# Optimization experiments

Measured on AMD Instinct MI355X. Metric: run time of the kernel, lower is better.

Reference implementation:

```python
import jax, jax.numpy as jnp
import numpy as np

N, E, T = 20000, 320000, 64
INP, EMB, OUT = 128, 16, 3
HEADS, MSIZE, MDIM, KDIM, VDIM = 4, 1024, 128, 64, 64


def setup_inputs() -> dict:
    key = jax.random.key(0)
    ks = iter(jax.random.split(key, 64))

    def nrm(shape, s=0.05):
        return jax.random.normal(next(ks), shape, dtype=jnp.float32) * s

    return dict(
        x=jax.random.normal(next(ks), (N, INP), dtype=jnp.float32),
        edge_index=jax.random.randint(next(ks), (2, E), 0, N),
        index=5,
        inp_types=jax.random.randint(next(ks), (T,), 0, 4),
        log_return=jax.random.normal(next(ks), (T,), dtype=jnp.float32),
        # SAGEConv 1 (SoftmaxAggregation temp t1, lin_l/lin_r, bias=False)
        t1=jnp.ones((1, INP), jnp.float32),
        W1l=nrm((INP, 512)), W1r=nrm((INP, 512)),
        ln1g_w=jnp.ones((512,), jnp.float32), ln1g_b=jnp.zeros((512,), jnp.float32),
        # SAGEConv 2
        t2=jnp.ones((1, 512), jnp.float32),
        W2l=nrm((512, 256)), W2r=nrm((512, 256)),
        ln2g_w=jnp.ones((256,), jnp.float32), ln2g_b=jnp.zeros((256,), jnp.float32),
        # MemPooling(256,128,heads=4,num_clusters=1)
        mp_k=nrm((HEADS, 1, 256), 1.0),
        mp_conv=nrm((HEADS,), 0.5),            # Conv2d(heads,1,1,bias=False)
        mp_lin=nrm((256, 128)),                # Linear(in,out,bias=False)
        fxg_w=nrm((128, 256)), fxg_b=jnp.zeros((256,), jnp.float32),
        # PolicyNet head
        emb=nrm((4, EMB), 1.0),
        fk_w=nrm((256, KDIM)), fk_b=jnp.zeros((KDIM,), jnp.float32),
        fv_w=nrm((256, VDIM)), fv_b=jnp.zeros((VDIM,), jnp.float32),
        # MultiHeadMemory
        mem=nrm((HEADS, MSIZE, MDIM), 1.0),
        mfk_w=nrm((MDIM, KDIM)), mfk_b=jnp.zeros((KDIM,), jnp.float32),
        mfv_w=nrm((MDIM, VDIM)), mfv_b=jnp.zeros((VDIM,), jnp.float32),
        mfx_w=nrm((VDIM * HEADS, VDIM)), mfx_b=jnp.zeros((VDIM,), jnp.float32),
        f1_w=nrm((INP + EMB + 2 * VDIM + 1, 512)),
        n1_w=jnp.ones((512,), jnp.float32), n1_b=jnp.zeros((512,), jnp.float32),
        f2_w=nrm((512, 256)),
        n2_w=jnp.ones((256,), jnp.float32), n2_b=jnp.zeros((256,), jnp.float32),
        f3_w=nrm((256, OUT)), f3_b=jnp.zeros((OUT,), jnp.float32),
    )


def _forward(x, t1, W1l, W1r, ln1g_w, ln1g_b, t2, W2l, W2r, ln2g_w, ln2g_b,
             mp_k, mp_conv, mp_lin, fxg_w, fxg_b, emb, fk_w, fk_b, fv_w, fv_b,
             mem, mfk_w, mfk_b, mfv_w, mfv_b, mfx_w, mfx_b,
             f1_w, n1_w, n1_b, f2_w, n2_w, n2_b, f3_w, f3_b,
             log_return, edge_index, inp_types, index):
    n = x.shape[0]
    src, dst = edge_index[0], edge_index[1]

    def sage(h, t, Wl, Wr):
        hj = h[src]                                    # [E, C] gather
        gate = hj * t                                  # learned softmax temperature
        m = jax.ops.segment_max(gate, dst, num_segments=n)
        e = jnp.exp(gate - m[dst])                     # segment-stable softmax
        s = jax.ops.segment_sum(e, dst, num_segments=n)
        agg = jax.ops.segment_sum(hj * (e / s[dst]), dst, num_segments=n)
        return agg @ Wl + h @ Wr                       # SAGEConv, bias=False

    def graph_ln(h, w, b, eps=1e-5):                   # PyG LayerNorm, mode='graph'
        hc = h - jnp.mean(h)
        return hc / jnp.sqrt(jnp.mean(hc * hc) + eps) * w + b

    h = jax.nn.relu(graph_ln(sage(x, t1, W1l, W1r), ln1g_w, ln1g_b))
    h = jax.nn.relu(graph_ln(sage(h, t2, W2l, W2r), ln2g_w, ln2g_b))

    # MemPooling (single graph => B=1), tau=1: student-t kernel over sq. distances
    H, K, C = mp_k.shape
    kk = mp_k.reshape(H * K, C)
    d2 = jnp.maximum(jnp.sum(kk * kk, 1)[:, None] - 2.0 * (kk @ h.T)
                     + jnp.sum(h * h, 1)[None, :], 0.0)        # [H*K, N]
    dist = 1.0 / (1.0 + d2)
    dist = dist.reshape(H, K, n).transpose(0, 2, 1)[None]      # [1, H, N, K]
    S = dist / jnp.sum(dist, -1, keepdims=True)
    S = jax.nn.softmax(jnp.einsum('h,bhnk->bnk', mp_conv, S), axis=-1)  # [1, N, K]
    zp = jnp.einsum('bnk,nc->bkc', S, h)[:, 0, :]              # squeeze(1), K==1
    z = (zp @ mp_lin) @ fxg_w + fxg_b                          # [1, 256]

    q = jax.nn.softmax(z @ fk_w + fk_b, axis=-1)               # [1, key_dim]
    v = z @ fv_w + fv_b                                        # [1, val_dim]

    # MultiHeadMemory
    km = jax.nn.softmax(mem @ mfk_w + mfk_b, axis=-1)          # [H, M, key]
    vm = mem @ mfv_w + mfv_b                                   # [H, M, val]
    w = jax.nn.softmax(jnp.einsum('bk,hnk->bhn', q, km), axis=-1)
    mv = jnp.einsum('bhn,hnv->bhv', w, vm).reshape(q.shape[0], -1)
    m_out = mv @ mfx_w + mfx_b                                 # [1, val]

    zz = jnp.concatenate([v, m_out], axis=-1)                  # [1, 2*val]
    t_len = inp_types.shape[0]
    xi = jnp.broadcast_to(x[index][None, :], (t_len, x.shape[1]))
    zb = jnp.broadcast_to(zz, (t_len, zz.shape[1]))
    feat = jnp.concatenate([xi, emb[inp_types], log_return.reshape(-1, 1), zb], axis=-1)

    def ln(h2, w2, b2, eps=1e-5):                              # nn.LayerNorm (last dim)
        mu = jnp.mean(h2, -1, keepdims=True)
        hc = h2 - mu
        return hc / jnp.sqrt(jnp.mean(hc * hc, -1, keepdims=True) + eps) * w2 + b2

    h1 = jax.nn.relu(ln(feat @ f1_w, n1_w, n1_b))              # dropout = identity (eval)
    h2 = jax.nn.relu(ln(h1 @ f2_w, n2_w, n2_b))
    return jax.nn.softmax(h2 @ f3_w + f3_b, axis=-1)           # [T, out_dim]


def reference(x, edge_index, index, inp_types, log_return, t1, W1l, W1r, ln1g_w, ln1g_b,
              t2, W2l, W2r, ln2g_w, ln2g_b, mp_k, mp_conv, mp_lin, fxg_w, fxg_b, emb,
              fk_w, fk_b, fv_w, fv_b, mem, mfk_w, mfk_b, mfv_w, mfv_b, mfx_w, mfx_b,
              f1_w, n1_w, n1_b, f2_w, n2_w, n2_b, f3_w, f3_b):
    return _forward(x, t1, W1l, W1r, ln1g_w, ln1g_b, t2, W2l, W2r, ln2g_w, ln2g_b,
                    mp_k, mp_conv, mp_lin, fxg_w, fxg_b, emb, fk_w, fk_b, fv_w, fv_b,
                    mem, mfk_w, mfk_b, mfv_w, mfv_b, mfx_w, mfx_b,
                    f1_w, n1_w, n1_b, f2_w, n2_w, n2_b, f3_w, f3_b,
                    log_return, edge_index, inp_types, index)
```

## Files before the change

kernel.cpp:

```cpp
#include <hip/hip_runtime.h>

typedef __attribute__((ext_vector_type(8))) short bf16x8;
typedef __attribute__((ext_vector_type(8))) unsigned short ushort8_t;
typedef __attribute__((ext_vector_type(4))) float f32x4;

__device__ __forceinline__ unsigned short f2bf(float f) {
    unsigned int x = __float_as_uint(f);
    unsigned int r = x + 0x7fffu + ((x >> 16) & 1u);
    return (unsigned short)(r >> 16);
}
__device__ __forceinline__ float bf2f(unsigned short u) {
    return __uint_as_float(((unsigned int)u) << 16);
}
__device__ __forceinline__ float fexp2(float x) { return __builtin_amdgcn_exp2f(x); }

#define LOG2E 1.44269504089f

__global__ __launch_bounds__(256) void prep_kernel(
    const int* __restrict__ dst, int E, int* __restrict__ counts,
    const float* __restrict__ x, unsigned short* __restrict__ xb, size_t nx4,
    const float* __restrict__ W1l, const float* __restrict__ W1r, unsigned short* __restrict__ Bt1,
    const float* __restrict__ W2l, const float* __restrict__ W2r, unsigned short* __restrict__ Bt2) {
    int i = blockIdx.x * 256 + threadIdx.x;
    int total = gridDim.x * 256;
    if (i < E) atomicAdd(&counts[dst[i]], 1);
    for (size_t j = i; j < nx4; j += total) {
        float4 v = *(const float4*)(x + j * 4);
        ushort4 o;
        o.x = f2bf(v.x); o.y = f2bf(v.y); o.z = f2bf(v.z); o.w = f2bf(v.w);
        *(ushort4*)(xb + j * 4) = o;
    }
    if (i < 512 * 256) {
        int nn = i >> 8, k = i & 255;
        float v = (k < 128) ? W1l[(size_t)k * 512 + nn] : W1r[(size_t)(k - 128) * 512 + nn];
        Bt1[i] = f2bf(v);
    }
    if (i < 256 * 1024) {
        int nn = i >> 10, k = i & 1023;
        float v = (k < 512) ? W2l[(size_t)k * 256 + nn] : W2r[(size_t)(k - 512) * 256 + nn];
        Bt2[i] = f2bf(v);
    }
}

template <int CHUNK>
__global__ __launch_bounds__(1024) void scan_kernel(int* __restrict__ cnt,
                                                    int* __restrict__ off, int n) {
    __shared__ int s[1024];
    int tid = threadIdx.x;
    int base = tid * CHUNK;
    int loc[CHUNK];
    int sum = 0;
#pragma unroll
    for (int i = 0; i < CHUNK; ++i) {
        int idx = base + i;
        int v = 0;
        if (idx < n) { v = cnt[idx]; cnt[idx] = 0; }
        sum += v;
        loc[i] = sum;
    }
    s[tid] = sum;
    __syncthreads();
    for (int d = 1; d < 1024; d <<= 1) {
        int t = (tid >= d) ? s[tid - d] : 0;
        __syncthreads();
        s[tid] += t;
        __syncthreads();
    }
    int prev = (tid > 0) ? s[tid - 1] : 0;
    if (tid == 0) off[0] = 0;
#pragma unroll
    for (int i = 0; i < CHUNK; ++i) {
        int idx = base + i;
        if (idx < n) off[idx + 1] = prev + loc[i];
    }
}

__global__ void fill_kernel(const int* __restrict__ src, const int* __restrict__ dst, int E,
                            const int* __restrict__ off, int* __restrict__ cursor,
                            int* __restrict__ srcs) {
    int i = blockIdx.x * 256 + threadIdx.x;
    if (i < E) {
        int d = dst[i];
        int p = atomicAdd(&cursor[d], 1);
        srcs[off[d] + p] = src[i];
    }
}

__global__ __launch_bounds__(256) void agg512(const unsigned short* __restrict__ h,
                                              const float* __restrict__ t,
                                              const int* __restrict__ off,
                                              const int* __restrict__ srcs,
                                              unsigned short* __restrict__ agg, int n) {
    int wid = threadIdx.x >> 6, lane = threadIdx.x & 63;
    int node = blockIdx.x * 4 + wid;
    if (node >= n) return;
    int beg = off[node], end = off[node + 1];
    int col = lane * 8;
    float tc[8], sE[8], sW[8];
#pragma unroll
    for (int i = 0; i < 8; ++i) { tc[i] = t[col + i] * LOG2E; sE[i] = 0.f; sW[i] = 0.f; }
#define P8(u)                                       \
    _Pragma("unroll") for (int i = 0; i < 8; ++i) { \
        float v = bf2f(u[i]);                       \
        float wv = fexp2(v * tc[i]);                \
        sE[i] += wv; sW[i] += v * wv;               \
    }
    int e = beg;
    for (; e + 2 <= end; e += 2) {
        int s0 = srcs[e], s1 = srcs[e + 1];
        ushort8_t u0 = *(const ushort8_t*)(h + (size_t)s0 * 512 + col);
        ushort8_t u1 = *(const ushort8_t*)(h + (size_t)s1 * 512 + col);
        P8(u0) P8(u1)
    }
    if (e < end) {
        int s0 = srcs[e];
        ushort8_t u0 = *(const ushort8_t*)(h + (size_t)s0 * 512 + col);
        P8(u0)
    }
#undef P8
    ushort8_t o;
#pragma unroll
    for (int i = 0; i < 8; ++i) o[i] = f2bf((end > beg) ? (sW[i] / sE[i]) : 0.f);
    *(ushort8_t*)(agg + (size_t)node * 512 + col) = o;
}

__global__ __launch_bounds__(256) void agg128(const unsigned short* __restrict__ h,
                                              const float* __restrict__ t,
                                              const int* __restrict__ off,
                                              const int* __restrict__ srcs,
                                              unsigned short* __restrict__ agg, int n) {
    int wid = threadIdx.x >> 6, lane = threadIdx.x & 63;
    int node = blockIdx.x * 4 + wid;
    if (node >= n) return;
    int beg = off[node], end = off[node + 1];
    int col = lane * 2;
    float t0 = t[col] * LOG2E, t1 = t[col + 1] * LOG2E;
    float e0 = 0.f, e1 = 0.f, w0 = 0.f, w1 = 0.f;
#define P2(u)                                          \
    {                                                  \
        float a = bf2f(u.x), b = bf2f(u.y);            \
        float xa = fexp2(a * t0), xb = fexp2(b * t1);  \
        e0 += xa; e1 += xb; w0 += a * xa; w1 += b * xb; \
    }
    int e = beg;
    for (; e + 4 <= end; e += 4) {
        ushort2 u0 = *(const ushort2*)(h + (size_t)srcs[e] * 128 + col);
        ushort2 u1 = *(const ushort2*)(h + (size_t)srcs[e + 1] * 128 + col);
        ushort2 u2 = *(const ushort2*)(h + (size_t)srcs[e + 2] * 128 + col);
        ushort2 u3 = *(const ushort2*)(h + (size_t)srcs[e + 3] * 128 + col);
        P2(u0) P2(u1) P2(u2) P2(u3)
    }
    for (; e < end; ++e) {
        ushort2 u0 = *(const ushort2*)(h + (size_t)srcs[e] * 128 + col);
        P2(u0)
    }
#undef P2
    ushort2 o;
    o.x = f2bf((end > beg) ? (w0 / e0) : 0.f);
    o.y = f2bf((end > beg) ? (w1 / e1) : 0.f);
    *(ushort2*)(agg + (size_t)node * 128 + col) = o;
}

__global__ __launch_bounds__(256) void gemm_dual_mfma3(
    const unsigned short* __restrict__ A1, const unsigned short* __restrict__ A2,
    const unsigned short* __restrict__ Bt,
    unsigned short* __restrict__ Cb, double* __restrict__ part,
    int M, int N, int K1, int K2) {
    const int Kc = K1 + K2;
    __shared__ unsigned short As[64 * 40];
    __shared__ unsigned short Bs[256 * 40];
    __shared__ double rs[256], rs2[256];
    int tid = threadIdx.x;
    int lane = tid & 63, w = tid >> 6;
    int m0 = blockIdx.y * 64, n0 = blockIdx.x * 256;
    f32x4 acc[4][4] = {};
    int kg = lane >> 4, lr = lane & 15;

    for (int k0 = 0; k0 < Kc; k0 += 32) {
        const unsigned short* Asrc;
        int kk, Ksrc;
        if (k0 < K1) { Asrc = A1; kk = k0; Ksrc = K1; }
        else         { Asrc = A2; kk = k0 - K1; Ksrc = K2; }
        {
            int r = tid >> 2, ch = tid & 3;
            int gr = m0 + r;
            ushort8_t v = {0, 0, 0, 0, 0, 0, 0, 0};
            if (gr < M) v = *(const ushort8_t*)(Asrc + (size_t)gr * Ksrc + kk + ch * 8);
            *(ushort8_t*)&As[r * 40 + ch * 8] = v;
        }
#pragma unroll
        for (int it = 0; it < 4; ++it) {
            int idx = tid + it * 256;
            int r = idx >> 2, ch = idx & 3;
            const unsigned short* srcp = Bt + (size_t)(n0 + r) * Kc + k0 + ch * 8;
            *(ushort8_t*)&Bs[r * 40 + ch * 8] = *(const ushort8_t*)srcp;
        }
        __syncthreads();
        bf16x8 a[4], b[4];
#pragma unroll
        for (int i = 0; i < 4; ++i)
            a[i] = *(bf16x8*)&As[(i * 16 + lr) * 40 + kg * 8];
#pragma unroll
        for (int j = 0; j < 4; ++j)
            b[j] = *(bf16x8*)&Bs[(w * 64 + j * 16 + lr) * 40 + kg * 8];
#pragma unroll
        for (int i = 0; i < 4; ++i)
#pragma unroll
            for (int j = 0; j < 4; ++j)
                acc[i][j] = __builtin_amdgcn_mfma_f32_16x16x32_bf16(a[i], b[j], acc[i][j], 0, 0, 0);
        __syncthreads();
    }
    double s = 0, s2 = 0;
#pragma unroll
    for (int i = 0; i < 4; ++i) {
        int rbase = m0 + i * 16 + kg * 4;
#pragma unroll
        for (int j = 0; j < 4; ++j) {
            int col = n0 + w * 64 + j * 16 + lr;
#pragma unroll
            for (int reg = 0; reg < 4; ++reg) {
                int row = rbase + reg;
                if (row < M) {
                    float v = acc[i][j][reg];
                    Cb[(size_t)row * N + col] = f2bf(v);
                    s += v;
                    s2 += (double)v * v;
                }
            }
        }
    }
    rs[tid] = s;
    rs2[tid] = s2;
    __syncthreads();
    for (int d = 128; d; d >>= 1) {
        if (tid < d) { rs[tid] += rs[tid + d]; rs2[tid] += rs2[tid + d]; }
        __syncthreads();
    }
    if (tid == 0) {
        int bid = blockIdx.y * gridDim.x + blockIdx.x;
        part[bid * 2] = rs[0];
        part[bid * 2 + 1] = rs2[0];
    }
}

template <int C>
__global__ __launch_bounds__(256) void ln_relu_ip(unsigned short* __restrict__ z,
                                                  const float* __restrict__ w,
                                                  const float* __restrict__ b,
                                                  const double* __restrict__ part, int nb,
                                                  float invn, size_t n) {
    __shared__ float st[2];
    if (threadIdx.x < 64) {
        double s = 0, s2 = 0;
        for (int i = threadIdx.x; i < nb; i += 64) { s += part[2 * i]; s2 += part[2 * i + 1]; }
        for (int d = 32; d; d >>= 1) { s += __shfl_down(s, d); s2 += __shfl_down(s2, d); }
        if (threadIdx.x == 0) {
            float mu = (float)(s * invn);
            float var = (float)(s2 * invn) - mu * mu;
            st[0] = mu;
            st[1] = rsqrtf(var + 1e-5f);
        }
    }
    __syncthreads();
    float mu = st[0], inv = st[1];
    size_t stride = (size_t)gridDim.x * 256 * 4;
    for (size_t i = ((size_t)blockIdx.x * 256 + threadIdx.x) * 4; i < n; i += stride) {
        ushort4 v = *(const ushort4*)(z + i);
        int c = (int)(i & (C - 1));
        ushort4 o;
        o.x = f2bf(fmaxf((bf2f(v.x) - mu) * inv * w[c] + b[c], 0.f));
        o.y = f2bf(fmaxf((bf2f(v.y) - mu) * inv * w[c + 1] + b[c + 1], 0.f));
        o.z = f2bf(fmaxf((bf2f(v.z) - mu) * inv * w[c + 2] + b[c + 2], 0.f));
        o.w = f2bf(fmaxf((bf2f(v.w) - mu) * inv * w[c + 3] + b[c + 3], 0.f));
        *(ushort4*)(z + i) = o;
    }
}

__global__ __launch_bounds__(256) void ln_colsum(const unsigned short* __restrict__ z2,
                                                 const float* __restrict__ w,
                                                 const float* __restrict__ b,
                                                 const double* __restrict__ part, int nb,
                                                 float invn, int n,
                                                 float* __restrict__ cspartT) {
    __shared__ float red[8 * 256];
    __shared__ float st[2];
    int tid = threadIdx.x;
    if (tid < 64) {
        double s = 0, s2 = 0;
        for (int i = tid; i < nb; i += 64) { s += part[2 * i]; s2 += part[2 * i + 1]; }
        for (int d = 32; d; d >>= 1) { s += __shfl_down(s, d); s2 += __shfl_down(s2, d); }
        if (tid == 0) {
            float mu = (float)(s * invn);
            float var = (float)(s2 * invn) - mu * mu;
            st[0] = mu;
            st[1] = rsqrtf(var + 1e-5f);
        }
    }
    __syncthreads();
    float mu = st[0], inv = st[1];
    int cg = tid & 31;
    int rl = tid >> 5;
    int c8 = cg * 8;
    float lw[8], lb[8];
#pragma unroll
    for (int i = 0; i < 8; ++i) { lw[i] = w[c8 + i] * inv; lb[i] = b[c8 + i] - mu * inv * w[c8 + i]; }
    int rows_per = (n + gridDim.x - 1) / gridDim.x;
    int r0 = blockIdx.x * rows_per;
    int r1 = min(n, r0 + rows_per);
    float acc[8] = {};
    for (int r = r0 + rl; r < r1; r += 8) {
        ushort8_t u = *(const ushort8_t*)(z2 + (size_t)r * 256 + c8);
#pragma unroll
        for (int i = 0; i < 8; ++i) acc[i] += fmaxf(bf2f(u[i]) * lw[i] + lb[i], 0.f);
    }
#pragma unroll
    for (int i = 0; i < 8; ++i) red[rl * 256 + c8 + i] = acc[i];
    __syncthreads();
    float s = 0;
#pragma unroll
    for (int r = 0; r < 8; ++r) s += red[r * 256 + tid];
    cspartT[tid * 64 + blockIdx.x] = s;
}

__global__ __launch_bounds__(256) void zqv_kernel(const float* __restrict__ cspartT,
                                                  const float* __restrict__ mp_lin,
                                                  const float* __restrict__ fxg_w,
                                                  const float* __restrict__ fxg_b,
                                                  const float* __restrict__ fk_w,
                                                  const float* __restrict__ fk_b,
                                                  const float* __restrict__ fv_w,
                                                  const float* __restrict__ fv_b,
                                                  float* __restrict__ qv) {
    __shared__ float zp_s[256], u_s[128], z_s[256], ql_s[64];
    __shared__ float part_s[1024];
    int tid = threadIdx.x;
    {
        float s = 0;
        const float* p = cspartT + tid * 64;
#pragma unroll
        for (int i = 0; i < 16; ++i) {
            float4 v = *(const float4*)(p + i * 4);
            s += v.x + v.y + v.z + v.w;
        }
        zp_s[tid] = s;
    }
    __syncthreads();
    {
        int og = tid & 31, kc = tid >> 5;
        int j4 = og * 4;
        f32x4 a = {0.f, 0.f, 0.f, 0.f};
        for (int ci = 0; ci < 32; ++ci) {
            int c = kc * 32 + ci;
            float4 w = *(const float4*)(mp_lin + (size_t)c * 128 + j4);
            float zc = zp_s[c];
            a[0] += zc * w.x; a[1] += zc * w.y; a[2] += zc * w.z; a[3] += zc * w.w;
        }
#pragma unroll
        for (int i = 0; i < 4; ++i) part_s[kc * 128 + j4 + i] = a[i];
    }
    __syncthreads();
    if (tid < 128) {
        float s = 0;
#pragma unroll
        for (int kc = 0; kc < 8; ++kc) s += part_s[kc * 128 + tid];
        u_s[tid] = s;
    }
    __syncthreads();
    {
        int og = tid & 63, kc = tid >> 6;
        int j4 = og * 4;
        f32x4 a = {0.f, 0.f, 0.f, 0.f};
        for (int ci = 0; ci < 32; ++ci) {
            int c = kc * 32 + ci;
            float4 w = *(const float4*)(fxg_w + (size_t)c * 256 + j4);
            float uc = u_s[c];
            a[0] += uc * w.x; a[1] += uc * w.y; a[2] += uc * w.z; a[3] += uc * w.w;
        }
#pragma unroll
        for (int i = 0; i < 4; ++i) part_s[kc * 256 + j4 + i] = a[i];
    }
    __syncthreads();
    {
        float s = fxg_b[tid];
#pragma unroll
        for (int kc = 0; kc < 4; ++kc) s += part_s[kc * 256 + tid];
        z_s[tid] = s;
    }
    __syncthreads();
    {
        int og = tid & 15, kc = tid >> 4;
        int j4 = og * 4;
        f32x4 a = {0.f, 0.f, 0.f, 0.f};
        for (int ci = 0; ci < 16; ++ci) {
            int c = kc * 16 + ci;
            float4 w = *(const float4*)(fk_w + (size_t)c * 64 + j4);
            float zc = z_s[c];
            a[0] += zc * w.x; a[1] += zc * w.y; a[2] += zc * w.z; a[3] += zc * w.w;
        }
#pragma unroll
        for (int i = 0; i < 4; ++i) part_s[kc * 64 + j4 + i] = a[i];
    }
    __syncthreads();
    if (tid < 64) {
        float s = fk_b[tid];
#pragma unroll
        for (int kc = 0; kc < 16; ++kc) s += part_s[kc * 64 + tid];
        ql_s[tid] = s;
    }
    __syncthreads();
    {
        int og = tid & 15, kc = tid >> 4;
        int j4 = og * 4;
        f32x4 a = {0.f, 0.f, 0.f, 0.f};
        for (int ci = 0; ci < 16; ++ci) {
            int c = kc * 16 + ci;
            float4 w = *(const float4*)(fv_w + (size_t)c * 64 + j4);
            float zc = z_s[c];
            a[0] += zc * w.x; a[1] += zc * w.y; a[2] += zc * w.z; a[3] += zc * w.w;
        }
#pragma unroll
        for (int i = 0; i < 4; ++i) part_s[kc * 64 + j4 + i] = a[i];
    }
    __syncthreads();
    if (tid < 64) {
        float mx = ql_s[tid];
        for (int d = 32; d; d >>= 1) mx = fmaxf(mx, __shfl_xor(mx, d));
        float e = __expf(ql_s[tid] - mx);
        float s = e;
        for (int d = 32; d; d >>= 1) s += __shfl_xor(s, d);
        qv[tid] = e / s;
        float vv = fv_b[tid];
#pragma unroll
        for (int kc = 0; kc < 16; ++kc) vv += part_s[kc * 64 + tid];
        qv[64 + tid] = vv;
    }
}

__global__ __launch_bounds__(256) void mem_kv_logit(const float* __restrict__ mem,
                                                    const float* __restrict__ mfk_w,
                                                    const float* __restrict__ mfk_b,
                                                    const float* __restrict__ mfv_w,
                                                    const float* __restrict__ mfv_b,
                                                    const float* __restrict__ qv,
                                                    float* __restrict__ logits,
                                                    float* __restrict__ vm) {
    __shared__ float rows[4][128];
    __shared__ float qs[64];
    int tid = threadIdx.x;
    int r0 = blockIdx.x * 4;
    if (tid < 64) qs[tid] = qv[tid];
    for (int i = tid; i < 512; i += 256) rows[i >> 7][i & 127] = mem[(size_t)r0 * 128 + i];
    __syncthreads();
    int lr = tid >> 6;
    int lane = tid & 63;
    const float* row = rows[lr];
    float kl = mfk_b[lane], vl = mfv_b[lane];
#pragma unroll 8
    for (int c = 0; c < 128; ++c) {
        float rv = row[c];
        kl += rv * mfk_w[c * 64 + lane];
        vl += rv * mfv_w[c * 64 + lane];
    }
    float mx = kl;
    for (int d = 32; d; d >>= 1) mx = fmaxf(mx, __shfl_xor(mx, d));
    float e = __expf(kl - mx);
    float s = e;
    for (int d = 32; d; d >>= 1) s += __shfl_xor(s, d);
    float kval = e / s;
    float wl = kval * qs[lane];
    for (int d = 32; d; d >>= 1) wl += __shfl_xor(wl, d);
    size_t gr = (size_t)(r0 + lr);
    if (lane == 0) logits[gr] = wl;
    vm[gr * 64 + lane] = vl;
}

__global__ __launch_bounds__(256) void attend_part(const float* __restrict__ logits,
                                                   const float* __restrict__ vm,
                                                   float* __restrict__ part) {
    int b = blockIdx.x;
    int h = b >> 4;
    int s0 = (b & 15) * 64;
    int tid = threadIdx.x;
    __shared__ float els[64];
    __shared__ float pr[4][64];
    __shared__ float lmax_s, lsum_s;
    if (tid < 64) {
        float lg = logits[h * 1024 + s0 + tid];
        float m = lg;
        for (int d = 32; d; d >>= 1) m = fmaxf(m, __shfl_xor(m, d));
        float e = __expf(lg - m);
        els[tid] = e;
        float s = e;
        for (int d = 32; d; d >>= 1) s += __shfl_xor(s, d);
        if (tid == 0) { lmax_s = m; lsum_s = s; }
    }
    __syncthreads();
    int dd = tid & 63, g = tid >> 6;
    float acc = 0;
    for (int s = g; s < 64; s += 4)
        acc += els[s] * vm[((size_t)h * 1024 + s0 + s) * 64 + dd];
    pr[g][dd] = acc;
    __syncthreads();
    if (tid < 64) {
        float pv = pr[0][tid] + pr[1][tid] + pr[2][tid] + pr[3][tid];
        part[b * 66 + 2 + tid] = pv;
        if (tid == 0) { part[b * 66] = lmax_s; part[b * 66 + 1] = lsum_s; }
    }
}

__global__ __launch_bounds__(256) void attend_final(const float* __restrict__ part,
                                                    const float* __restrict__ mfx_w,
                                                    const float* __restrict__ mfx_b,
                                                    float* __restrict__ m_out) {
    __shared__ float mv[256];
    __shared__ float part_s[1024];
    int tid = threadIdx.x;
    int h = tid >> 6, dd = tid & 63;
    float gmax = -1e30f;
#pragma unroll
    for (int p = 0; p < 16; ++p) gmax = fmaxf(gmax, part[(h * 16 + p) * 66]);
    float total = 0.f, acc = 0.f;
#pragma unroll
    for (int p = 0; p < 16; ++p) {
        float sc = __expf(part[(h * 16 + p) * 66] - gmax);
        total += part[(h * 16 + p) * 66 + 1] * sc;
        acc += part[(h * 16 + p) * 66 + 2 + dd] * sc;
    }
    mv[h * 64 + dd] = acc / total;
    __syncthreads();
    {
        int og = tid & 15, kc = tid >> 4;
        int j4 = og * 4;
        f32x4 a = {0.f, 0.f, 0.f, 0.f};
        for (int ci = 0; ci < 16; ++ci) {
            int c = kc * 16 + ci;
            float4 w = *(const float4*)(mfx_w + (size_t)c * 64 + j4);
            float mc = mv[c];
            a[0] += mc * w.x; a[1] += mc * w.y; a[2] += mc * w.z; a[3] += mc * w.w;
        }
#pragma unroll
        for (int i = 0; i < 4; ++i) part_s[kc * 64 + j4 + i] = a[i];
    }
    __syncthreads();
    if (tid < 64) {
        float s = mfx_b[tid];
#pragma unroll
        for (int kc = 0; kc < 16; ++kc) s += part_s[kc * 64 + tid];
        m_out[tid] = s;
    }
}

__device__ __forceinline__ float block_sum_256(float v, float* red) {
    int tid = threadIdx.x;
    red[tid] = v;
    __syncthreads();
    for (int d = 128; d; d >>= 1) { if (tid < d) red[tid] += red[tid + d]; __syncthreads(); }
    float r = red[0];
    __syncthreads();
    return r;
}

__global__ __launch_bounds__(256) void head_kernel(
    const float* __restrict__ x, const int* __restrict__ index_p,
    const int* __restrict__ inp_types, const float* __restrict__ log_return,
    const float* __restrict__ emb, const float* __restrict__ qv,
    const float* __restrict__ m_out, const float* __restrict__ f1_w,
    const float* __restrict__ n1_w, const float* __restrict__ n1_b,
    const float* __restrict__ f2_w, const float* __restrict__ n2_w,
    const float* __restrict__ n2_b, const float* __restrict__ f3_w,
    const float* __restrict__ f3_b, float* __restrict__ out) {
    __shared__ float feat[273];
    __shared__ float h1[512];
    __shared__ float h2[256];
    __shared__ float red[256];
    __shared__ float l3[3];
    int r = blockIdx.x, tid = threadIdx.x;
    int idx = index_p[0];
    for (int i = tid; i < 273; i += 256) {
        float val;
        if (i < 128) val = x[(size_t)idx * 128 + i];
        else if (i < 144) val = emb[inp_types[r] * 16 + (i - 128)];
        else if (i == 144) val = log_return[r];
        else if (i < 209) val = qv[64 + (i - 145)];
        else val = m_out[i - 209];
        feat[i] = val;
    }
    __syncthreads();
    float a0 = 0, a1 = 0;
    for (int c = 0; c < 273; ++c) {
        float f = feat[c];
        a0 += f * f1_w[c * 512 + tid];
        a1 += f * f1_w[c * 512 + tid + 256];
    }
    float mu = block_sum_256(a0 + a1, red) / 512.f;
    float c0 = a0 - mu, c1 = a1 - mu;
    float var = block_sum_256(c0 * c0 + c1 * c1, red) / 512.f;
    float inv = rsqrtf(var + 1e-5f);
    h1[tid] = fmaxf(c0 * inv * n1_w[tid] + n1_b[tid], 0.f);
    h1[tid + 256] = fmaxf(c1 * inv * n1_w[tid + 256] + n1_b[tid + 256], 0.f);
    __syncthreads();
    float b0 = 0;
    for (int c = 0; c < 512; ++c) b0 += h1[c] * f2_w[c * 256 + tid];
    float mu2 = block_sum_256(b0, red) / 256.f;
    float cc = b0 - mu2;
    float var2 = block_sum_256(cc * cc, red) / 256.f;
    float inv2 = rsqrtf(var2 + 1e-5f);
    h2[tid] = fmaxf(cc * inv2 * n2_w[tid] + n2_b[tid], 0.f);
    __syncthreads();
    if (tid < 3) {
        float a = f3_b[tid];
        for (int c = 0; c < 256; ++c) a += h2[c] * f3_w[c * 3 + tid];
        l3[tid] = a;
    }
    __syncthreads();
    if (tid < 3) {
        float mx = fmaxf(l3[0], fmaxf(l3[1], l3[2]));
        float s = __expf(l3[0] - mx) + __expf(l3[1] - mx) + __expf(l3[2] - mx);
        out[r * 3 + tid] = __expf(l3[tid] - mx) / s;
    }
}

extern "C" void kernel_launch(void* const* d_in, const int* in_sizes, int n_in,
                              void* d_out, int out_size, void* d_ws, size_t ws_size,
                              hipStream_t stream) {
    const float* x = (const float*)d_in[0];
    const int* ei = (const int*)d_in[1];
    const int* index_p = (const int*)d_in[2];
    const int* inp_types = (const int*)d_in[3];
    const float* log_return = (const float*)d_in[4];
    const float* t1 = (const float*)d_in[5];
    const float* W1l = (const float*)d_in[6];
    const float* W1r = (const float*)d_in[7];
    const float* ln1g_w = (const float*)d_in[8];
    const float* ln1g_b = (const float*)d_in[9];
    const float* t2 = (const float*)d_in[10];
    const float* W2l = (const float*)d_in[11];
    const float* W2r = (const float*)d_in[12];
    const float* ln2g_w = (const float*)d_in[13];
    const float* ln2g_b = (const float*)d_in[14];
    const float* mp_lin = (const float*)d_in[17];
    const float* fxg_w = (const float*)d_in[18];
    const float* fxg_b = (const float*)d_in[19];
    const float* emb = (const float*)d_in[20];
    const float* fk_w = (const float*)d_in[21];
    const float* fk_b = (const float*)d_in[22];
    const float* fv_w = (const float*)d_in[23];
    const float* fv_b = (const float*)d_in[24];
    const float* mem = (const float*)d_in[25];
    const float* mfk_w = (const float*)d_in[26];
    const float* mfk_b = (const float*)d_in[27];
    const float* mfv_w = (const float*)d_in[28];
    const float* mfv_b = (const float*)d_in[29];
    const float* mfx_w = (const float*)d_in[30];
    const float* mfx_b = (const float*)d_in[31];
    const float* f1_w = (const float*)d_in[32];
    const float* n1_w = (const float*)d_in[33];
    const float* n1_b = (const float*)d_in[34];
    const float* f2_w = (const float*)d_in[35];
    const float* n2_w = (const float*)d_in[36];
    const float* n2_b = (const float*)d_in[37];
    const float* f3_w = (const float*)d_in[38];
    const float* f3_b = (const float*)d_in[39];
    float* out = (float*)d_out;

    int n = in_sizes[0] / 128;
    int E = in_sizes[1] / 2;
    int T = in_sizes[3];
    const int* src = ei;
    const int* dst = ei + E;

    char* w = (char*)d_ws;
    auto alloc = [&](size_t bytes) {
        char* p = w;
        w += (bytes + 255) & ~(size_t)255;
        return p;
    };
    int* counts = (int*)alloc((size_t)n * 4);
    int* off = (int*)alloc((size_t)(n + 1) * 4);
    int* srcs = (int*)alloc((size_t)E * 4);
    unsigned short* xb = (unsigned short*)alloc((size_t)n * 128 * 2);
    unsigned short* agg1b = (unsigned short*)alloc((size_t)n * 128 * 2);
    unsigned short* z1b = (unsigned short*)alloc((size_t)n * 512 * 2);
    unsigned short* agg2b = (unsigned short*)alloc((size_t)n * 512 * 2);
    unsigned short* z2b = (unsigned short*)alloc((size_t)n * 256 * 2);
    double* partd = (double*)alloc(2048 * 2 * 8);
    float* cspartT = (float*)alloc(256 * 64 * 4);
    float* qv = (float*)alloc(128 * 4);
    float* logits = (float*)alloc((size_t)4 * 1024 * 4);
    float* vm = (float*)alloc((size_t)4 * 1024 * 64 * 4);
    float* apart = (float*)alloc(64 * 66 * 4);
    float* m_out = (float*)alloc(64 * 4);
    unsigned short* Bt1 = (unsigned short*)alloc((size_t)512 * 256 * 2);
    unsigned short* Bt2 = (unsigned short*)alloc((size_t)256 * 1024 * 2);

    int nblk_e = (E + 255) / 256;
    int mblk64 = (n + 63) / 64;

    hipMemsetAsync(counts, 0, (size_t)n * 4, stream);
    prep_kernel<<<nblk_e, 256, 0, stream>>>(dst, E, counts, x, xb, (size_t)n * 128 / 4,
                                            W1l, W1r, Bt1, W2l, W2r, Bt2);
    scan_kernel<20><<<1, 1024, 0, stream>>>(counts, off, n);
    fill_kernel<<<nblk_e, 256, 0, stream>>>(src, dst, E, off, counts, srcs);

    agg128<<<(n + 3) / 4, 256, 0, stream>>>(xb, t1, off, srcs, agg1b, n);
    gemm_dual_mfma3<<<dim3(2, mblk64), 256, 0, stream>>>(agg1b, xb, Bt1, z1b, partd, n, 512, 128, 128);
    ln_relu_ip<512><<<1024, 256, 0, stream>>>(z1b, ln1g_w, ln1g_b, partd, 2 * mblk64,
                                              1.0f / ((float)n * 512.f), (size_t)n * 512);

    agg512<<<(n + 3) / 4, 256, 0, stream>>>(z1b, t2, off, srcs, agg2b, n);
    gemm_dual_mfma3<<<dim3(1, mblk64), 256, 0, stream>>>(agg2b, z1b, Bt2, z2b, partd, n, 256, 512, 512);

    ln_colsum<<<64, 256, 0, stream>>>(z2b, ln2g_w, ln2g_b, partd, mblk64,
                                      1.0f / ((float)n * 256.f), n, cspartT);
    zqv_kernel<<<1, 256, 0, stream>>>(cspartT, mp_lin, fxg_w, fxg_b, fk_w, fk_b, fv_w, fv_b, qv);

    mem_kv_logit<<<1024, 256, 0, stream>>>(mem, mfk_w, mfk_b, mfv_w, mfv_b, qv, logits, vm);
    attend_part<<<64, 256, 0, stream>>>(logits, vm, apart);
    attend_final<<<1, 256, 0, stream>>>(apart, mfx_w, mfx_b, m_out);

    head_kernel<<<T, 256, 0, stream>>>(x, index_p, inp_types, log_return, emb, qv, m_out,
                                       f1_w, n1_w, n1_b, f2_w, n2_w, n2_b, f3_w, f3_b, out);
}
```

Measured before the change: 290.5 us.

## Split agg512 columns across two grid halves and fold attend_final into head

The 512-wide softmax aggregation now splits columns across a second grid dimension. Each wave handles 4 columns per lane instead of 8 and unrolls the edge loop by 4, which doubles the wave count and puts more gathers in flight. The attend_final reduction is also merged into head_kernel so that one launch is removed. The cost is that every head block (64 of them) redundantly recomputes the memory-attention merge, and src indices are loaded twice across the two column halves.

```diff
diff --git a/kernel.cpp b/kernel.cpp
--- a/kernel.cpp
+++ b/kernel.cpp
@@ -86,42 +86,48 @@
     }
 }
 
-__global__ __launch_bounds__(256) void agg512(const unsigned short* __restrict__ h,
-                                              const float* __restrict__ t,
-                                              const int* __restrict__ off,
-                                              const int* __restrict__ srcs,
-                                              unsigned short* __restrict__ agg, int n) {
+__global__ __launch_bounds__(256) void agg512s(const unsigned short* __restrict__ h,
+                                               const float* __restrict__ t,
+                                               const int* __restrict__ off,
+                                               const int* __restrict__ srcs,
+                                               unsigned short* __restrict__ agg, int n) {
     int wid = threadIdx.x >> 6, lane = threadIdx.x & 63;
     int node = blockIdx.x * 4 + wid;
     if (node >= n) return;
     int beg = off[node], end = off[node + 1];
-    int col = lane * 8;
-    float tc[8], sE[8], sW[8];
-#pragma unroll
-    for (int i = 0; i < 8; ++i) { tc[i] = t[col + i] * LOG2E; sE[i] = 0.f; sW[i] = 0.f; }
-#define P8(u)                                       \
-    _Pragma("unroll") for (int i = 0; i < 8; ++i) { \
-        float v = bf2f(u[i]);                       \
-        float wv = fexp2(v * tc[i]);                \
-        sE[i] += wv; sW[i] += v * wv;               \
+    int col = blockIdx.y * 256 + lane * 4;
+    float tc0 = t[col] * LOG2E, tc1 = t[col + 1] * LOG2E;
+    float tc2 = t[col + 2] * LOG2E, tc3 = t[col + 3] * LOG2E;
+    float sE0 = 0.f, sE1 = 0.f, sE2 = 0.f, sE3 = 0.f;
+    float sW0 = 0.f, sW1 = 0.f, sW2 = 0.f, sW3 = 0.f;
+#define P4(u)                                                        \
+    {                                                                \
+        float v0 = bf2f(u.x), v1 = bf2f(u.y);                        \
+        float v2 = bf2f(u.z), v3 = bf2f(u.w);                        \
+        float w0_ = fexp2(v0 * tc0), w1_ = fexp2(v1 * tc1);          \
+        float w2_ = fexp2(v2 * tc2), w3_ = fexp2(v3 * tc3);          \
+        sE0 += w0_; sW0 += v0 * w0_; sE1 += w1_; sW1 += v1 * w1_;    \
+        sE2 += w2_; sW2 += v2 * w2_; sE3 += w3_; sW3 += v3 * w3_;    \
     }
     int e = beg;
-    for (; e + 2 <= end; e += 2) {
-        int s0 = srcs[e], s1 = srcs[e + 1];
-        ushort8_t u0 = *(const ushort8_t*)(h + (size_t)s0 * 512 + col);
-        ushort8_t u1 = *(const ushort8_t*)(h + (size_t)s1 * 512 + col);
-        P8(u0) P8(u1)
-    }
-    if (e < end) {
-        int s0 = srcs[e];
-        ushort8_t u0 = *(const ushort8_t*)(h + (size_t)s0 * 512 + col);
-        P8(u0)
-    }
-#undef P8
-    ushort8_t o;
-#pragma unroll
-    for (int i = 0; i < 8; ++i) o[i] = f2bf((end > beg) ? (sW[i] / sE[i]) : 0.f);
-    *(ushort8_t*)(agg + (size_t)node * 512 + col) = o;
+    for (; e + 4 <= end; e += 4) {
+        ushort4 u0 = *(const ushort4*)(h + (size_t)srcs[e] * 512 + col);
+        ushort4 u1 = *(const ushort4*)(h + (size_t)srcs[e + 1] * 512 + col);
+        ushort4 u2 = *(const ushort4*)(h + (size_t)srcs[e + 2] * 512 + col);
+        ushort4 u3 = *(const ushort4*)(h + (size_t)srcs[e + 3] * 512 + col);
+        P4(u0) P4(u1) P4(u2) P4(u3)
+    }
+    for (; e < end; ++e) {
+        ushort4 u0 = *(const ushort4*)(h + (size_t)srcs[e] * 512 + col);
+        P4(u0)
+    }
+#undef P4
+    ushort4 o;
+    o.x = f2bf((end > beg) ? (sW0 / sE0) : 0.f);
+    o.y = f2bf((end > beg) ? (sW1 / sE1) : 0.f);
+    o.z = f2bf((end > beg) ? (sW2 / sE2) : 0.f);
+    o.w = f2bf((end > beg) ? (sW3 / sE3) : 0.f);
+    *(ushort4*)(agg + (size_t)node * 512 + col) = o;
 }
 
 __global__ __launch_bounds__(256) void agg128(const unsigned short* __restrict__ h,
@@ -508,48 +514,6 @@
     }
 }
 
-__global__ __launch_bounds__(256) void attend_final(const float* __restrict__ part,
-                                                    const float* __restrict__ mfx_w,
-                                                    const float* __restrict__ mfx_b,
-                                                    float* __restrict__ m_out) {
-    __shared__ float mv[256];
-    __shared__ float part_s[1024];
-    int tid = threadIdx.x;
-    int h = tid >> 6, dd = tid & 63;
-    float gmax = -1e30f;
-#pragma unroll
-    for (int p = 0; p < 16; ++p) gmax = fmaxf(gmax, part[(h * 16 + p) * 66]);
-    float total = 0.f, acc = 0.f;
-#pragma unroll
-    for (int p = 0; p < 16; ++p) {
-        float sc = __expf(part[(h * 16 + p) * 66] - gmax);
-        total += part[(h * 16 + p) * 66 + 1] * sc;
-        acc += part[(h * 16 + p) * 66 + 2 + dd] * sc;
-    }
-    mv[h * 64 + dd] = acc / total;
-    __syncthreads();
-    {
-        int og = tid & 15, kc = tid >> 4;
-        int j4 = og * 4;
-        f32x4 a = {0.f, 0.f, 0.f, 0.f};
-        for (int ci = 0; ci < 16; ++ci) {
-            int c = kc * 16 + ci;
-            float4 w = *(const float4*)(mfx_w + (size_t)c * 64 + j4);
-            float mc = mv[c];
-            a[0] += mc * w.x; a[1] += mc * w.y; a[2] += mc * w.z; a[3] += mc * w.w;
-        }
-#pragma unroll
-        for (int i = 0; i < 4; ++i) part_s[kc * 64 + j4 + i] = a[i];
-    }
-    __syncthreads();
-    if (tid < 64) {
-        float s = mfx_b[tid];
-#pragma unroll
-        for (int kc = 0; kc < 16; ++kc) s += part_s[kc * 64 + tid];
-        m_out[tid] = s;
-    }
-}
-
 __device__ __forceinline__ float block_sum_256(float v, float* red) {
     int tid = threadIdx.x;
     red[tid] = v;
@@ -564,7 +528,8 @@
     const float* __restrict__ x, const int* __restrict__ index_p,
     const int* __restrict__ inp_types, const float* __restrict__ log_return,
     const float* __restrict__ emb, const float* __restrict__ qv,
-    const float* __restrict__ m_out, const float* __restrict__ f1_w,
+    const float* __restrict__ apart, const float* __restrict__ mfx_w,
+    const float* __restrict__ mfx_b, const float* __restrict__ f1_w,
     const float* __restrict__ n1_w, const float* __restrict__ n1_b,
     const float* __restrict__ f2_w, const float* __restrict__ n2_w,
     const float* __restrict__ n2_b, const float* __restrict__ f3_w,
@@ -574,15 +539,54 @@
     __shared__ float h2[256];
     __shared__ float red[256];
     __shared__ float l3[3];
+    __shared__ float mv_s[256];
+    __shared__ float mpart[1024];
+    __shared__ float m_out_s[64];
     int r = blockIdx.x, tid = threadIdx.x;
     int idx = index_p[0];
+    {
+        int h = tid >> 6, dd = tid & 63;
+        float gmax = -1e30f;
+#pragma unroll
+        for (int p = 0; p < 16; ++p) gmax = fmaxf(gmax, apart[(h * 16 + p) * 66]);
+        float total = 0.f, acc = 0.f;
+#pragma unroll
+        for (int p = 0; p < 16; ++p) {
+            float sc = __expf(apart[(h * 16 + p) * 66] - gmax);
+            total += apart[(h * 16 + p) * 66 + 1] * sc;
+            acc += apart[(h * 16 + p) * 66 + 2 + dd] * sc;
+        }
+        mv_s[h * 64 + dd] = acc / total;
+    }
+    __syncthreads();
+    {
+        int og = tid & 15, kc = tid >> 4;
+        int j4 = og * 4;
+        f32x4 a = {0.f, 0.f, 0.f, 0.f};
+        for (int ci = 0; ci < 16; ++ci) {
+            int c = kc * 16 + ci;
+            float4 w = *(const float4*)(mfx_w + (size_t)c * 64 + j4);
+            float mc = mv_s[c];
+            a[0] += mc * w.x; a[1] += mc * w.y; a[2] += mc * w.z; a[3] += mc * w.w;
+        }
+#pragma unroll
+        for (int i = 0; i < 4; ++i) mpart[kc * 64 + j4 + i] = a[i];
+    }
+    __syncthreads();
+    if (tid < 64) {
+        float s = mfx_b[tid];
+#pragma unroll
+        for (int kc = 0; kc < 16; ++kc) s += mpart[kc * 64 + tid];
+        m_out_s[tid] = s;
+    }
+    __syncthreads();
     for (int i = tid; i < 273; i += 256) {
         float val;
         if (i < 128) val = x[(size_t)idx * 128 + i];
         else if (i < 144) val = emb[inp_types[r] * 16 + (i - 128)];
         else if (i == 144) val = log_return[r];
         else if (i < 209) val = qv[64 + (i - 145)];
-        else val = m_out[i - 209];
+        else val = m_out_s[i - 209];
         feat[i] = val;
     }
     __syncthreads();
@@ -689,7 +693,6 @@
     float* logits = (float*)alloc((size_t)4 * 1024 * 4);
     float* vm = (float*)alloc((size_t)4 * 1024 * 64 * 4);
     float* apart = (float*)alloc(64 * 66 * 4);
-    float* m_out = (float*)alloc(64 * 4);
     unsigned short* Bt1 = (unsigned short*)alloc((size_t)512 * 256 * 2);
     unsigned short* Bt2 = (unsigned short*)alloc((size_t)256 * 1024 * 2);
 
@@ -707,7 +710,7 @@
     ln_relu_ip<512><<<1024, 256, 0, stream>>>(z1b, ln1g_w, ln1g_b, partd, 2 * mblk64,
                                               1.0f / ((float)n * 512.f), (size_t)n * 512);
 
-    agg512<<<(n + 3) / 4, 256, 0, stream>>>(z1b, t2, off, srcs, agg2b, n);
+    agg512s<<<dim3((n + 3) / 4, 2), 256, 0, stream>>>(z1b, t2, off, srcs, agg2b, n);
     gemm_dual_mfma3<<<dim3(1, mblk64), 256, 0, stream>>>(agg2b, z1b, Bt2, z2b, partd, n, 256, 512, 512);
 
     ln_colsum<<<64, 256, 0, stream>>>(z2b, ln2g_w, ln2g_b, partd, mblk64,
@@ -716,8 +719,8 @@
 
     mem_kv_logit<<<1024, 256, 0, stream>>>(mem, mfk_w, mfk_b, mfv_w, mfv_b, qv, logits, vm);
     attend_part<<<64, 256, 0, stream>>>(logits, vm, apart);
-    attend_final<<<1, 256, 0, stream>>>(apart, mfx_w, mfx_b, m_out);
-
-    head_kernel<<<T, 256, 0, stream>>>(x, index_p, inp_types, log_return, emb, qv, m_out,
-                                       f1_w, n1_w, n1_b, f2_w, n2_w, n2_b, f3_w, f3_b, out);
-}
+
+    head_kernel<<<T, 256, 0, stream>>>(x, index_p, inp_types, log_return, emb, qv, apart,
+                                       mfx_w, mfx_b, f1_w, n1_w, n1_b, f2_w, n2_w, n2_b,
+                                       f3_w, f3_b, out);
+}
```

New measurement: 287.2 us (median of 2 runs). Within noise of the previous version (-1.1%).
